# Optimization experiments

Hardware: AMD Instinct MI355X
Metric: run time of the kernel (lower is better)

The kernel has to match this reference:

```python
import jax, jax.numpy as jnp
import numpy as np

B, N, F, D, M, R, K, TOPR = 32, 1024, 10, 64, 4, 8, 20, 2
TAU = 1.0
BN_EPS = 1e-5


def setup_inputs() -> dict:
    key = jax.random.key(0)
    ks = jax.random.split(key, 20)
    s = 0.1
    p = {}
    p['data'] = jax.random.normal(ks[0], (B, N, F), jnp.float32)
    u = jnp.clip(jax.random.uniform(ks[1], (B, M), jnp.float32), 1e-6, 1.0 - 1e-6)
    p['gumbel_noise'] = -jnp.log(-jnp.log(u))
    p['W_cond'] = jax.random.normal(ks[2], (F, D), jnp.float32) * s
    p['b_cond'] = jnp.zeros((D,), jnp.float32)
    p['W_ap'] = jax.random.normal(ks[3], (D, D), jnp.float32) * s
    p['b_ap'] = jnp.zeros((D,), jnp.float32)
    p['W_av'] = jax.random.normal(ks[4], (D, 1), jnp.float32) * s
    p['W_r'] = jax.random.normal(ks[5], (D, M), jnp.float32) * s
    p['b_r'] = jnp.zeros((M,), jnp.float32)
    p['e_base'] = jax.random.normal(ks[6], (N, D), jnp.float32) * s
    p['lr_u'] = jax.random.normal(ks[7], (M, N, R), jnp.float32) * s
    p['lr_v'] = jax.random.normal(ks[8], (M, R, D), jnp.float32) * s
    p['W_gnn'] = jax.random.normal(ks[9], (F, D), jnp.float32) * s
    p['att_i'] = jax.random.normal(ks[10], (D,), jnp.float32) * s
    p['att_j'] = jax.random.normal(ks[11], (D,), jnp.float32) * s
    p['att_em_i'] = jax.random.normal(ks[12], (D,), jnp.float32) * s
    p['att_em_j'] = jax.random.normal(ks[13], (D,), jnp.float32) * s
    p['b_gnn'] = jnp.zeros((D,), jnp.float32)
    p['bn1_gamma'] = jnp.ones((D,), jnp.float32)
    p['bn1_beta'] = jnp.zeros((D,), jnp.float32)
    p['node_embed_table'] = jax.random.normal(ks[14], (N, D), jnp.float32) * s
    p['bn_out_gamma'] = jnp.ones((D,), jnp.float32)
    p['bn_out_beta'] = jnp.zeros((D,), jnp.float32)
    p['W_out'] = jax.random.normal(ks[15], (D, 1), jnp.float32) * s
    p['b_out'] = jnp.zeros((1,), jnp.float32)
    return p


def _nan(x):
    return jnp.nan_to_num(x, nan=0.0, posinf=1e4, neginf=-1e4)


def _bn(x, gamma, beta, axes):
    # BatchNorm1d in training mode: biased batch stats over `axes`.
    mu = x.mean(axes, keepdims=True)
    var = x.var(axes, keepdims=True)
    return (x - mu) * jax.lax.rsqrt(var + BN_EPS) * gamma + beta


def reference(data, gumbel_noise, W_cond, b_cond, W_ap, b_ap, W_av, W_r, b_r,
              e_base, lr_u, lr_v, W_gnn, att_i, att_j, att_em_i, att_em_j,
              b_gnn, bn1_gamma, bn1_beta, node_embed_table,
              bn_out_gamma, bn_out_beta, W_out, b_out):
    x_det = jax.lax.stop_gradient(data)                      # data.clone().detach()
    # --- condition attention pooling ---
    h_it = data @ W_cond + b_cond                            # [B,N,D]
    ah = jax.nn.leaky_relu(h_it @ W_ap + b_ap, 0.2)
    e_it = _nan((ah @ W_av)[..., 0])                         # [B,N]
    beta = jax.nn.softmax(e_it, axis=1)
    h_sys = jnp.sum(beta[..., None] * h_it, axis=1)          # [B,D]
    # --- gumbel top-k routing with straight-through ---
    pi_soft = jax.nn.softmax((h_sys @ W_r + b_r + gumbel_noise) / TAU, axis=-1)
    topv, topi = jax.lax.top_k(pi_soft, TOPR)
    pi_hard = jnp.sum(jax.nn.one_hot(topi, M, dtype=pi_soft.dtype) * topv[..., None], axis=1)
    pi_hard = pi_hard / jnp.maximum(pi_hard.sum(-1, keepdims=True), 1e-12)
    pi_t = jax.lax.stop_gradient(pi_hard - pi_soft) + pi_soft
    # --- low-rank expert prototypes -> mixed node embeddings ---
    proto = e_base[None] + jnp.einsum('mnr,mrd->mnd', lr_u, lr_v)    # [M,N,D]
    mixed = _nan(jnp.einsum('bm,mnd->bnd', pi_t, proto))             # [B,N,D]
    # --- dynamic top-k graph construction ---
    scores = _nan(jnp.einsum('bid,bjd->bij', mixed, mixed))          # [B,N,N]
    topk_vals, topk_idx = jax.lax.top_k(scores, K)                   # src nodes per dst: [B,N,K]
    topk_w = jax.nn.softmax(topk_vals, axis=-1)                      # edge weights
    # --- GAT-style layer with embedding-augmented keys, self loops re-added ---
    x_lin = x_det @ W_gnn                                            # [B,N,D]
    s_i = x_lin @ att_i + mixed @ att_em_i                           # [B,N]
    s_j = x_lin @ att_j + mixed @ att_em_j
    sj_nb = jnp.take_along_axis(s_j, topk_idx.reshape(B, N * K), axis=1).reshape(B, N, K)
    self_mask = topk_idx == jnp.arange(N)[None, :, None]             # remove_self_loops on topk edges
    alpha_nb = jnp.where(self_mask, -jnp.inf, jax.nn.leaky_relu(s_i[:, :, None] + sj_nb, 0.2))
    alpha_self = jax.nn.leaky_relu(s_i + s_j, 0.2)
    att = jax.nn.softmax(jnp.concatenate([alpha_nb, alpha_self[..., None]], axis=-1), axis=-1)
    w_nb = att[..., :K] * topk_w                                     # edge_weight modulation
    w_self = att[..., K]
    x_src = jnp.take_along_axis(x_lin, topk_idx.reshape(B, N * K)[..., None], axis=1).reshape(B, N, K, D)
    gnn = jnp.einsum('bnk,bnkd->bnd', w_nb, x_src) + w_self[..., None] * x_lin + b_gnn
    gnn = jax.nn.relu(_bn(gnn.reshape(B * N, D), bn1_gamma, bn1_beta, 0).reshape(B, N, D))
    # --- output head ---
    out = gnn * node_embed_table[None]                               # [B,N,D]
    out = jax.nn.relu(_bn(out, bn_out_gamma, bn_out_beta, (0, 1)))   # dropout = identity (eval)
    out = (out @ W_out + b_out).reshape(-1, N)                       # [B,N]
    return out, h_sys, pi_soft
```

## Files before the change

kernel.cpp:

```cpp
#include <hip/hip_runtime.h>
#include <math.h>

#define BB 32
#define NN 1024
#define FF 10
#define DD 64
#define MM 4
#define RR 8
#define KK 20
#define BNROWS (BB*NN)

#define OFF_HIT   0ull
#define OFF_XLIN  2097152ull
#define OFF_EIT   4194304ull
#define OFF_PIT   4227072ull
#define OFF_MIXED 4227200ull
#define OFF_SI    6324352ull
#define OFF_SJ    6357120ull
#define OFF_GNN   7700608ull
#define OFF_OUTP  9797760ull
#define OFF_STAT  11894912ull
#define OFF_SC    (OFF_STAT + 2560ull)

__device__ __forceinline__ float wave_sum(float v) {
    #pragma unroll
    for (int off = 32; off; off >>= 1) v += __shfl_xor(v, off);
    return v;
}
__device__ __forceinline__ float wave_max(float v) {
    #pragma unroll
    for (int off = 32; off; off >>= 1) v = fmaxf(v, __shfl_xor(v, off));
    return v;
}

__global__ __launch_bounds__(256) void k_rows(
    const float* __restrict__ data, const float* __restrict__ W_cond,
    const float* __restrict__ b_cond, const float* __restrict__ W_ap,
    const float* __restrict__ b_ap, const float* __restrict__ W_av,
    const float* __restrict__ W_gnn,
    float* __restrict__ h_it, float* __restrict__ x_lin, float* __restrict__ e_it,
    float* __restrict__ stats)
{
    if (blockIdx.x < 10) {
        int idx = blockIdx.x * 256 + threadIdx.x;
        if (idx < 2336) stats[idx] = 0.f;
    }
    int w = threadIdx.x >> 6, lane = threadIdx.x & 63;
    int r = blockIdx.x * 4 + w;
    const float* dr = data + r * FF;
    float df[FF];
    #pragma unroll
    for (int f = 0; f < FF; f++) df[f] = dr[f];
    float h = b_cond[lane], x = 0.f;
    #pragma unroll
    for (int f = 0; f < FF; f++) {
        h = fmaf(df[f], W_cond[f * DD + lane], h);
        x = fmaf(df[f], W_gnn[f * DD + lane], x);
    }
    h_it[r * DD + lane] = h;
    x_lin[r * DD + lane] = x;
    float acc = b_ap[lane];
    #pragma unroll
    for (int e2 = 0; e2 < DD; e2++)
        acc = fmaf(__shfl(h, e2), W_ap[e2 * DD + lane], acc);
    float lr = acc > 0.f ? acc : 0.2f * acc;
    float ep = wave_sum(lr * W_av[lane]);
    if (lane == 0) e_it[r] = ep;
}

__global__ __launch_bounds__(256) void k_pool2(
    const float* __restrict__ e_it, const float* __restrict__ h_it,
    float* __restrict__ num, float* __restrict__ den)
{
    int w = threadIdx.x >> 6, lane = threadIdx.x & 63;
    int b = blockIdx.x >> 3, ch = blockIdx.x & 7;
    int base = b * NN + ch * 128 + w * 32;
    float acc = 0.f, dn = 0.f;
    #pragma unroll 4
    for (int i = 0; i < 32; i++) {
        float e = e_it[base + i];
        float wgt = expf(e);
        acc = fmaf(wgt, h_it[(size_t)(base + i) * DD + lane], acc);
        dn += wgt;
    }
    __shared__ float pa[4][DD];
    __shared__ float pd[4];
    pa[w][lane] = acc;
    if (lane == 0) pd[w] = dn;
    __syncthreads();
    if (w == 0) {
        float s = pa[0][lane] + pa[1][lane] + pa[2][lane] + pa[3][lane];
        atomicAdd(&num[b * DD + lane], s);
        if (lane == 0) atomicAdd(&den[b], pd[0] + pd[1] + pd[2] + pd[3]);
    }
}

__global__ void k_route(const float* __restrict__ num, const float* __restrict__ den,
                        const float* __restrict__ W_r, const float* __restrict__ b_r,
                        const float* __restrict__ gumbel,
                        float* __restrict__ h_sys, float* __restrict__ pi_soft,
                        float* __restrict__ pi_t)
{
    int tid = threadIdx.x;
    for (int i = tid; i < BB * DD; i += 256)
        h_sys[i] = num[i] / den[i >> 6];
    if (tid >= BB) return;
    int b = tid;
    float inv = 1.0f / den[b];
    float lg[MM];
    #pragma unroll
    for (int m = 0; m < MM; m++) lg[m] = b_r[m] + gumbel[b * MM + m];
    for (int d = 0; d < DD; d++) {
        float hv = num[b * DD + d] * inv;
        #pragma unroll
        for (int m = 0; m < MM; m++) lg[m] = fmaf(hv, W_r[d * MM + m], lg[m]);
    }
    float mx = fmaxf(fmaxf(lg[0], lg[1]), fmaxf(lg[2], lg[3]));
    float s = 0.f, p[MM];
    #pragma unroll
    for (int m = 0; m < MM; m++) { p[m] = expf(lg[m] - mx); s += p[m]; }
    #pragma unroll
    for (int m = 0; m < MM; m++) { p[m] /= s; pi_soft[b * MM + m] = p[m]; }
    int i1 = 0; float v1 = p[0];
    #pragma unroll
    for (int m = 1; m < MM; m++) if (p[m] > v1) { v1 = p[m]; i1 = m; }
    int i2 = -1; float v2 = -1.f;
    #pragma unroll
    for (int m = 0; m < MM; m++) if (m != i1 && p[m] > v2) { v2 = p[m]; i2 = m; }
    float norm = fmaxf(v1 + v2, 1e-12f);
    #pragma unroll
    for (int m = 0; m < MM; m++)
        pi_t[b * MM + m] = (m == i1 ? v1 : (m == i2 ? v2 : 0.f)) / norm;
}

__global__ __launch_bounds__(256) void k_mixed(
    const float* __restrict__ e_base, const float* __restrict__ lr_u,
    const float* __restrict__ lr_v, const float* __restrict__ pi_t,
    const float* __restrict__ x_lin,
    const float* __restrict__ att_i, const float* __restrict__ att_j,
    const float* __restrict__ att_em_i, const float* __restrict__ att_em_j,
    float* __restrict__ mixed, float* __restrict__ s_i, float* __restrict__ s_j)
{
    int w = threadIdx.x >> 6, lane = threadIdx.x & 63;
    int r = blockIdx.x * 4 + w;
    int b = r >> 10, n = r & 1023;
    float LR[MM];
    #pragma unroll
    for (int m = 0; m < MM; m++) {
        float a = 0.f;
        #pragma unroll
        for (int rr = 0; rr < RR; rr++)
            a = fmaf(lr_u[(m * NN + n) * RR + rr], lr_v[(m * RR + rr) * DD + lane], a);
        LR[m] = a;
    }
    float eb = e_base[n * DD + lane];
    float mx = 0.f;
    #pragma unroll
    for (int m = 0; m < MM; m++) mx = fmaf(pi_t[b * MM + m], eb + LR[m], mx);
    mixed[(size_t)r * DD + lane] = mx;
    float x = x_lin[(size_t)r * DD + lane];
    float r1 = wave_sum(x * att_i[lane] + mx * att_em_i[lane]);
    float r2 = wave_sum(x * att_j[lane] + mx * att_em_j[lane]);
    if (lane == 0) { s_i[r] = r1; s_j[r] = r2; }
}

__global__ __launch_bounds__(256) void k_score(
    const float* __restrict__ mixed_chunk, float* __restrict__ sc)
{
    __shared__ float As[32 * 132];
    __shared__ float Bs[32 * 132];
    int t = threadIdx.x;
    int bb = blockIdx.x >> 6;
    int rr = blockIdx.x & 63;
    int it = rr >> 3, jt = rr & 7;
    int i0 = it * 128, j0 = jt * 128;
    const float* mb = mixed_chunk + (size_t)bb * NN * DD;

    int tx = t & 15, ty = t >> 4;
    float acc[8][8];
    #pragma unroll
    for (int a = 0; a < 8; a++)
        #pragma unroll
        for (int bj = 0; bj < 8; bj++) acc[a][bj] = 0.f;

    int rowi[4], qi[4], swi[4];
    #pragma unroll
    for (int c = 0; c < 4; c++) {
        int id = t + c * 256;
        rowi[c] = (id & 15) | ((id >> 7) << 4);
        qi[c] = (id >> 4) & 7;
        swi[c] = ((rowi[c] & 4) << 4) | ((rowi[c] >> 3) << 2) | (rowi[c] & 3);
    }

    float4 pa[4], pb[4];
    #pragma unroll
    for (int c = 0; c < 4; c++) {
        pa[c] = *(const float4*)(mb + (size_t)(i0 + rowi[c]) * DD + qi[c] * 4);
        pb[c] = *(const float4*)(mb + (size_t)(j0 + rowi[c]) * DD + qi[c] * 4);
    }
    for (int hh = 0; hh < 2; hh++) {
        if (hh) __syncthreads();
        #pragma unroll
        for (int c = 0; c < 4; c++) {
            int pos = qi[c] * 4 * 132 + swi[c];
            As[pos] = pa[c].x; As[pos + 132] = pa[c].y; As[pos + 264] = pa[c].z; As[pos + 396] = pa[c].w;
            Bs[pos] = pb[c].x; Bs[pos + 132] = pb[c].y; Bs[pos + 264] = pb[c].z; Bs[pos + 396] = pb[c].w;
        }
        __syncthreads();
        if (hh == 0) {
            #pragma unroll
            for (int c = 0; c < 4; c++) {
                pa[c] = *(const float4*)(mb + (size_t)(i0 + rowi[c]) * DD + 32 + qi[c] * 4);
                pb[c] = *(const float4*)(mb + (size_t)(j0 + rowi[c]) * DD + 32 + qi[c] * 4);
            }
        }
        #pragma unroll 4
        for (int d = 0; d < 32; d++) {
            float4 a0 = *(const float4*)&As[d * 132 + ty * 4];
            float4 a1 = *(const float4*)&As[d * 132 + 64 + ty * 4];
            float4 b0 = *(const float4*)&Bs[d * 132 + tx * 4];
            float4 b1 = *(const float4*)&Bs[d * 132 + 64 + tx * 4];
            float av[8] = {a0.x, a0.y, a0.z, a0.w, a1.x, a1.y, a1.z, a1.w};
            float bv[8] = {b0.x, b0.y, b0.z, b0.w, b1.x, b1.y, b1.z, b1.w};
            #pragma unroll
            for (int a = 0; a < 8; a++)
                #pragma unroll
                for (int bj = 0; bj < 8; bj++)
                    acc[a][bj] = fmaf(av[a], bv[bj], acc[a][bj]);
        }
    }

    float* out = sc + ((size_t)bb * NN + i0 + ty * 8) * NN + j0 + tx * 8;
    #pragma unroll
    for (int a = 0; a < 8; a++) {
        float4 o0 = {acc[a][0], acc[a][1], acc[a][2], acc[a][3]};
        float4 o1 = {acc[a][4], acc[a][5], acc[a][6], acc[a][7]};
        *(float4*)(out + (size_t)a * NN) = o0;
        *(float4*)(out + (size_t)a * NN + 4) = o1;
    }
}

__global__ __launch_bounds__(256) void k_selgat(
    const float* __restrict__ sc, int b0,
    const float* __restrict__ x_lin, const float* __restrict__ s_i,
    const float* __restrict__ s_j, const float* __restrict__ b_gnn,
    float* __restrict__ gnn_pre)
{
    int w = threadIdx.x >> 6, lane = threadIdx.x & 63;
    int lr = blockIdx.x * 4 + w;
    int r = b0 * NN + lr;
    int b = r >> 10, n = r & 1023;
    const float* row = sc + (size_t)lr * NN;

    unsigned uk[16];
    #pragma unroll
    for (int c = 0; c < 4; c++) {
        float4 v = *(const float4*)(row + c * 256 + lane * 4);
        float vv[4] = {v.x, v.y, v.z, v.w};
        #pragma unroll
        for (int q = 0; q < 4; q++) {
            unsigned u = __float_as_uint(vv[q]);
            uk[c * 4 + q] = u ^ (((unsigned)((int)u >> 31)) | 0x80000000u);
        }
    }
    unsigned mx = uk[0];
    #pragma unroll
    for (int i = 1; i < 16; i++) mx = uk[i] > mx ? uk[i] : mx;
    unsigned sv = mx;
    #pragma unroll
    for (int blk = 2; blk <= 64; blk <<= 1) {
        #pragma unroll
        for (int dist = blk >> 1; dist >= 1; dist >>= 1) {
            unsigned pv = (unsigned)__shfl_xor((int)sv, dist);
            bool up = (lane & blk) == 0;
            bool upper = (lane & dist) == 0;
            bool g = sv > pv;
            sv = (((g == upper) == up)) ? sv : pv;
        }
    }
    unsigned tau = (unsigned)__shfl((int)sv, 19);

    __shared__ unsigned skey[4][64];
    __shared__ int sjj[4][64];
    int base = 0;
    #pragma unroll
    for (int s = 0; s < 16; s++) {
        bool q = uk[s] >= tau;
        unsigned long long m = __ballot(q);
        if (q) {
            int pos = base + __popcll(m & ((1ull << lane) - 1ull));
            if (pos < 64) {
                skey[w][pos] = uk[s];
                sjj[w][pos] = ((s >> 2) << 8) + lane * 4 + (s & 3);
            }
        }
        base += __popcll(m);
    }
    int C = base;

    float vk = -INFINITY; int ik = 0;
    if (C <= 64) {
        unsigned ck = 0u; int cj = 0x7FFFFFFF;
        if (lane < C) { ck = skey[w][lane]; cj = sjj[w][lane]; }
        if (C <= 32) {
            #pragma unroll
            for (int blk = 2; blk <= 32; blk <<= 1)
                #pragma unroll
                for (int dist = blk >> 1; dist >= 1; dist >>= 1) {
                    unsigned pk = (unsigned)__shfl_xor((int)ck, dist);
                    int pj = __shfl_xor(cj, dist);
                    bool up = (lane & blk) == 0;
                    bool upper = (lane & dist) == 0;
                    bool g = (ck > pk) || (ck == pk && cj < pj);
                    bool keep = ((g == upper) == up);
                    ck = keep ? ck : pk; cj = keep ? cj : pj;
                }
        } else {
            #pragma unroll
            for (int blk = 2; blk <= 64; blk <<= 1)
                #pragma unroll
                for (int dist = blk >> 1; dist >= 1; dist >>= 1) {
                    unsigned pk = (unsigned)__shfl_xor((int)ck, dist);
                    int pj = __shfl_xor(cj, dist);
                    bool up = (lane & blk) == 0;
                    bool upper = (lane & dist) == 0;
                    bool g = (ck > pk) || (ck == pk && cj < pj);
                    bool keep = ((g == upper) == up);
                    ck = keep ? ck : pk; cj = keep ? cj : pj;
                }
        }
        if (lane < KK) {
            unsigned u = (ck & 0x80000000u) ? (ck ^ 0x80000000u) : ~ck;
            vk = __uint_as_float(u);
            ik = cj;
        }
    } else {
        for (int k = 0; k < KK; k++) {
            unsigned bm = uk[0]; int bsl = 0;
            #pragma unroll
            for (int i = 1; i < 16; i++) if (uk[i] > bm) { bm = uk[i]; bsl = i; }
            unsigned wm = bm;
            #pragma unroll
            for (int off = 32; off; off >>= 1) {
                unsigned tt = (unsigned)__shfl_xor((int)wm, off);
                wm = tt > wm ? tt : wm;
            }
            unsigned long long ball = __ballot(bm == wm);
            int winner = (int)__builtin_ctzll(ball);
            int slotw = __shfl(bsl, winner);
            int jw = ((slotw >> 2) << 8) + winner * 4 + (slotw & 3);
            unsigned u2 = (wm & 0x80000000u) ? (wm ^ 0x80000000u) : ~wm;
            if (lane == k) { vk = __uint_as_float(u2); ik = jw; }
            if (lane == winner) uk[bsl] = 0u;
        }
    }

    float m1 = wave_max(vk);
    float ek = (lane < KK) ? expf(vk - m1) : 0.f;
    float s1v = wave_sum(ek);
    float wk = ek / s1v;
    float si = s_i[r], sjn = s_j[r];
    float a = -INFINITY;
    if (lane < KK) {
        float sjk = s_j[(b << 10) + ik];
        float t2 = si + sjk;
        a = (ik == n) ? -INFINITY : (t2 > 0.f ? t2 : 0.2f * t2);
    }
    float ts = si + sjn;
    float aself = ts > 0.f ? ts : 0.2f * ts;
    float am = wave_max(fmaxf(a, aself));
    float ea = (lane < KK && a != -INFINITY) ? expf(a - am) : 0.f;
    float es = expf(aself - am);
    float ssum = wave_sum(ea) + es;
    float wnb = (ea / ssum) * wk;
    float wself = es / ssum;
    float acc = b_gnn[lane] + wself * x_lin[(size_t)r * DD + lane];
    #pragma unroll
    for (int k = 0; k < KK; k++) {
        int jk = __shfl(ik, k);
        float wv = __shfl(wnb, k);
        acc = fmaf(wv, x_lin[((size_t)(b << 10) + jk) * DD + lane], acc);
    }
    gnn_pre[(size_t)r * DD + lane] = acc;
}

__global__ __launch_bounds__(256) void k_stats(const float* __restrict__ src, float* __restrict__ sums)
{
    int w = threadIdx.x >> 6, lane = threadIdx.x & 63;
    __shared__ float ps[4][DD], pq[4][DD];
    float s = 0.f, q = 0.f;
    int base = blockIdx.x * 128;
    for (int i = w; i < 128; i += 4) {
        float v = src[(size_t)(base + i) * DD + lane];
        s += v; q = fmaf(v, v, q);
    }
    ps[w][lane] = s; pq[w][lane] = q;
    __syncthreads();
    if (w == 0) {
        s = ps[0][lane] + ps[1][lane] + ps[2][lane] + ps[3][lane];
        q = pq[0][lane] + pq[1][lane] + pq[2][lane] + pq[3][lane];
        atomicAdd(&sums[lane], s);
        atomicAdd(&sums[DD + lane], q);
    }
}

__global__ __launch_bounds__(256) void k_bn1(
    const float* __restrict__ gnn_pre, float* __restrict__ stats,
    const float* __restrict__ gamma, const float* __restrict__ beta,
    const float* __restrict__ net, float* __restrict__ out_pre)
{
    int tid = threadIdx.x;
    int d0 = (tid & 15) * 4;
    float mean4[4], rs4[4], bt4[4];
    #pragma unroll
    for (int k = 0; k < 4; k++) {
        float mu = stats[d0 + k] * (1.0f / BNROWS);
        float var = stats[64 + d0 + k] * (1.0f / BNROWS) - mu * mu;
        mean4[k] = mu;
        rs4[k] = rsqrtf(var + 1e-5f) * gamma[d0 + k];
        bt4[k] = beta[d0 + k];
    }
    float s4[4] = {0, 0, 0, 0}, q4[4] = {0, 0, 0, 0};
    size_t base4 = (size_t)blockIdx.x * 2048;
    #pragma unroll
    for (int i = 0; i < 8; i++) {
        size_t f4 = base4 + (size_t)i * 256 + tid;
        float4 v = ((const float4*)gnn_pre)[f4];
        int n = ((int)(f4 >> 4)) & 1023;
        float4 nv = ((const float4*)net)[(size_t)n * 16 + (tid & 15)];
        float vv[4] = {v.x, v.y, v.z, v.w};
        float nn2[4] = {nv.x, nv.y, nv.z, nv.w};
        float ov[4];
        #pragma unroll
        for (int k = 0; k < 4; k++) {
            float y = (vv[k] - mean4[k]) * rs4[k] + bt4[k];
            y = y > 0.f ? y : 0.f;
            float o = y * nn2[k];
            ov[k] = o;
            s4[k] += o;
            q4[k] = fmaf(o, o, q4[k]);
        }
        float4 o4 = {ov[0], ov[1], ov[2], ov[3]};
        ((float4*)out_pre)[f4] = o4;
    }
    __shared__ float4 ls[256], lq[256];
    ls[tid] = make_float4(s4[0], s4[1], s4[2], s4[3]);
    lq[tid] = make_float4(q4[0], q4[1], q4[2], q4[3]);
    __syncthreads();
    if (tid < 16) {
        float4 S = ls[tid], Q = lq[tid];
        #pragma unroll
        for (int rr = 1; rr < 16; rr++) {
            float4 a = ls[tid + 16 * rr], b = lq[tid + 16 * rr];
            S.x += a.x; S.y += a.y; S.z += a.z; S.w += a.w;
            Q.x += b.x; Q.y += b.y; Q.z += b.z; Q.w += b.w;
        }
        atomicAdd(&stats[128 + tid * 4 + 0], S.x);
        atomicAdd(&stats[128 + tid * 4 + 1], S.y);
        atomicAdd(&stats[128 + tid * 4 + 2], S.z);
        atomicAdd(&stats[128 + tid * 4 + 3], S.w);
        atomicAdd(&stats[192 + tid * 4 + 0], Q.x);
        atomicAdd(&stats[192 + tid * 4 + 1], Q.y);
        atomicAdd(&stats[192 + tid * 4 + 2], Q.z);
        atomicAdd(&stats[192 + tid * 4 + 3], Q.w);
    }
}

__global__ __launch_bounds__(256) void k_head(
    const float* __restrict__ out_pre, const float* __restrict__ stats,
    const float* __restrict__ gamma, const float* __restrict__ beta,
    const float* __restrict__ W_out, const float* __restrict__ b_out,
    float* __restrict__ out)
{
    int w = threadIdx.x >> 6, lane = threadIdx.x & 63;
    int r = blockIdx.x * 4 + w;
    float mean = stats[lane] * (1.0f / BNROWS);
    float var = stats[DD + lane] * (1.0f / BNROWS) - mean * mean;
    float rs = rsqrtf(var + 1e-5f);
    float y = (out_pre[(size_t)r * DD + lane] - mean) * rs * gamma[lane] + beta[lane];
    y = y > 0.f ? y : 0.f;
    float p = wave_sum(y * W_out[lane]);
    if (lane == 0) out[r] = p + b_out[0];
}

extern "C" void kernel_launch(void* const* d_in, const int* in_sizes, int n_in,
                              void* d_out, int out_size, void* d_ws, size_t ws_size,
                              hipStream_t stream)
{
    const float* data     = (const float*)d_in[0];
    const float* gumbel   = (const float*)d_in[1];
    const float* W_cond   = (const float*)d_in[2];
    const float* b_cond   = (const float*)d_in[3];
    const float* W_ap     = (const float*)d_in[4];
    const float* b_ap     = (const float*)d_in[5];
    const float* W_av     = (const float*)d_in[6];
    const float* W_r      = (const float*)d_in[7];
    const float* b_r      = (const float*)d_in[8];
    const float* e_base   = (const float*)d_in[9];
    const float* lr_u     = (const float*)d_in[10];
    const float* lr_v     = (const float*)d_in[11];
    const float* W_gnn    = (const float*)d_in[12];
    const float* att_i    = (const float*)d_in[13];
    const float* att_j    = (const float*)d_in[14];
    const float* att_em_i = (const float*)d_in[15];
    const float* att_em_j = (const float*)d_in[16];
    const float* b_gnn    = (const float*)d_in[17];
    const float* bn1_g    = (const float*)d_in[18];
    const float* bn1_b    = (const float*)d_in[19];
    const float* net      = (const float*)d_in[20];
    const float* bno_g    = (const float*)d_in[21];
    const float* bno_b    = (const float*)d_in[22];
    const float* W_out    = (const float*)d_in[23];
    const float* b_out    = (const float*)d_in[24];

    float* ws = (float*)d_ws;
    float* h_it   = ws + OFF_HIT;
    float* x_lin  = ws + OFF_XLIN;
    float* e_it   = ws + OFF_EIT;
    float* pi_t   = ws + OFF_PIT;
    float* mixed  = ws + OFF_MIXED;
    float* s_i    = ws + OFF_SI;
    float* s_j    = ws + OFF_SJ;
    float* gnn_pre = ws + OFF_GNN;
    float* out_pre = ws + OFF_OUTP;
    float* stats   = ws + OFF_STAT;
    float* pnum    = stats + 256;
    float* pden    = stats + 2304;

    float* out0    = (float*)d_out;
    float* h_sys   = out0 + BB * NN;
    float* pi_soft = out0 + BB * NN + BB * DD;

    k_rows<<<BNROWS / 4, 256, 0, stream>>>(data, W_cond, b_cond, W_ap, b_ap, W_av, W_gnn,
                                           h_it, x_lin, e_it, stats);
    k_pool2<<<BB * 8, 256, 0, stream>>>(e_it, h_it, pnum, pden);
    k_route<<<1, 256, 0, stream>>>(pnum, pden, W_r, b_r, gumbel, h_sys, pi_soft, pi_t);
    k_mixed<<<BNROWS / 4, 256, 0, stream>>>(e_base, lr_u, lr_v, pi_t, x_lin,
                                            att_i, att_j, att_em_i, att_em_j, mixed, s_i, s_j);

    size_t ws_floats = ws_size / 4;
    size_t avail = ws_floats > OFF_SC ? ws_floats - OFF_SC : 0;
    int cb = (int)(avail / (size_t)(NN * NN));
    if (cb > BB) cb = BB;
    float* sc = ws + OFF_SC;
    if (cb < 1) { cb = 2; sc = h_it; }
    for (int b0 = 0; b0 < BB; b0 += cb) {
        int c = (BB - b0) < cb ? (BB - b0) : cb;
        k_score<<<c * 64, 256, 0, stream>>>(mixed + (size_t)b0 * NN * DD, sc);
        k_selgat<<<c * 256, 256, 0, stream>>>(sc, b0, x_lin, s_i, s_j, b_gnn, gnn_pre);
    }

    k_stats<<<256, 256, 0, stream>>>(gnn_pre, stats);
    k_bn1<<<256, 256, 0, stream>>>(gnn_pre, stats, bn1_g, bn1_b, net, out_pre);
    k_head<<<BNROWS / 4, 256, 0, stream>>>(out_pre, stats + 128, bno_g, bno_b, W_out, b_out, out0);
}
```

Measured before the change: 319.8 us.

## Fuse whole pipeline into one cooperative persistent kernel with grid syncs

Replaces the sequence of separate kernel launches with a single cooperative kernel on a fixed grid of 512 blocks. Stages are separated by grid-wide syncs, and grid-stride loops process rows and tiles. BN1 statistics are now accumulated inside the selection/GAT stage instead of a separate stats pass, and the fallback path gets the same fusion. This removes launch gaps and one full read of gnn_pre, at the cost of fewer blocks per stage, lower occupancy under launch bounds of (256,2), and several grid.sync barriers.

```diff
diff --git a/kernel.cpp b/kernel.cpp
--- a/kernel.cpp
+++ b/kernel.cpp
@@ -1,5 +1,8 @@
 #include <hip/hip_runtime.h>
+#include <hip/hip_cooperative_groups.h>
 #include <math.h>
+
+namespace cg = cooperative_groups;
 
 #define BB 32
 #define NN 1024
@@ -9,6 +12,7 @@
 #define RR 8
 #define KK 20
 #define BNROWS (BB*NN)
+#define GRID 512
 
 #define OFF_HIT   0ull
 #define OFF_XLIN  2097152ull
@@ -22,6 +26,16 @@
 #define OFF_STAT  11894912ull
 #define OFF_SC    (OFF_STAT + 2560ull)
 
+struct MegaArgs {
+    const float *data, *gumbel, *W_cond, *b_cond, *W_ap, *b_ap, *W_av, *W_r, *b_r,
+                *e_base, *lr_u, *lr_v, *W_gnn, *att_i, *att_j, *att_em_i, *att_em_j,
+                *b_gnn, *bn1_g, *bn1_b, *net, *bno_g, *bno_b, *W_out, *b_out;
+    float* ws;
+    float* out0;
+    float* sc;
+    int cb;
+};
+
 __device__ __forceinline__ float wave_sum(float v) {
     #pragma unroll
     for (int off = 32; off; off >>= 1) v += __shfl_xor(v, off);
@@ -31,6 +45,442 @@
     #pragma unroll
     for (int off = 32; off; off >>= 1) v = fmaxf(v, __shfl_xor(v, off));
     return v;
+}
+
+__global__ __launch_bounds__(256, 2) void k_mega(MegaArgs a)
+{
+    cg::grid_group grid = cg::this_grid();
+    __shared__ __align__(16) float smem[8448];
+
+    int t = threadIdx.x, w = t >> 6, lane = t & 63;
+    int blk = blockIdx.x;
+    int nb = gridDim.x;
+    int nwaves = nb * 4;
+    int gw = blk * 4 + w;
+
+    float* ws      = a.ws;
+    float* h_it    = ws + OFF_HIT;
+    float* x_lin   = ws + OFF_XLIN;
+    float* e_it    = ws + OFF_EIT;
+    float* pi_t    = ws + OFF_PIT;
+    float* mixed   = ws + OFF_MIXED;
+    float* s_i     = ws + OFF_SI;
+    float* s_j     = ws + OFF_SJ;
+    float* gnn_pre = ws + OFF_GNN;
+    float* out_pre = ws + OFF_OUTP;
+    float* stats   = ws + OFF_STAT;
+    float* pnum    = stats + 256;
+    float* pden    = stats + 2304;
+    float* out0    = a.out0;
+    float* h_sys   = out0 + BB * NN;
+    float* pi_soft = out0 + BB * NN + BB * DD;
+
+    if (blk == 0)
+        for (int idx = t; idx < 2336; idx += 256) stats[idx] = 0.f;
+    for (int r = gw; r < BNROWS; r += nwaves) {
+        const float* dr = a.data + r * FF;
+        float df[FF];
+        #pragma unroll
+        for (int f = 0; f < FF; f++) df[f] = dr[f];
+        float h = a.b_cond[lane], x = 0.f;
+        #pragma unroll
+        for (int f = 0; f < FF; f++) {
+            h = fmaf(df[f], a.W_cond[f * DD + lane], h);
+            x = fmaf(df[f], a.W_gnn[f * DD + lane], x);
+        }
+        h_it[r * DD + lane] = h;
+        x_lin[r * DD + lane] = x;
+        float acc = a.b_ap[lane];
+        #pragma unroll
+        for (int e2 = 0; e2 < DD; e2++)
+            acc = fmaf(__shfl(h, e2), a.W_ap[e2 * DD + lane], acc);
+        float lr2 = acc > 0.f ? acc : 0.2f * acc;
+        float ep = wave_sum(lr2 * a.W_av[lane]);
+        if (lane == 0) e_it[r] = ep;
+    }
+    grid.sync();
+
+    for (int ch = blk; ch < 256; ch += nb) {
+        __syncthreads();
+        int b = ch >> 3, c8 = ch & 7;
+        int base = b * NN + c8 * 128 + w * 32;
+        float accp = 0.f, dn = 0.f;
+        #pragma unroll 4
+        for (int i = 0; i < 32; i++) {
+            float e = e_it[base + i];
+            float wgt = expf(e);
+            accp = fmaf(wgt, h_it[(size_t)(base + i) * DD + lane], accp);
+            dn += wgt;
+        }
+        float* pa = smem;
+        float* pd = smem + 256;
+        pa[w * 64 + lane] = accp;
+        if (lane == 0) pd[w] = dn;
+        __syncthreads();
+        if (w == 0) {
+            float s = pa[lane] + pa[64 + lane] + pa[128 + lane] + pa[192 + lane];
+            atomicAdd(&pnum[b * DD + lane], s);
+            if (lane == 0) atomicAdd(&pden[b], pd[0] + pd[1] + pd[2] + pd[3]);
+        }
+    }
+    grid.sync();
+
+    if (blk == 0) {
+        for (int i = t; i < BB * DD; i += 256)
+            h_sys[i] = pnum[i] / pden[i >> 6];
+        if (t < BB) {
+            int b = t;
+            float inv = 1.0f / pden[b];
+            float lg[MM];
+            #pragma unroll
+            for (int m = 0; m < MM; m++) lg[m] = a.b_r[m] + a.gumbel[b * MM + m];
+            for (int d = 0; d < DD; d++) {
+                float hv = pnum[b * DD + d] * inv;
+                #pragma unroll
+                for (int m = 0; m < MM; m++) lg[m] = fmaf(hv, a.W_r[d * MM + m], lg[m]);
+            }
+            float mx = fmaxf(fmaxf(lg[0], lg[1]), fmaxf(lg[2], lg[3]));
+            float s = 0.f, p[MM];
+            #pragma unroll
+            for (int m = 0; m < MM; m++) { p[m] = expf(lg[m] - mx); s += p[m]; }
+            #pragma unroll
+            for (int m = 0; m < MM; m++) { p[m] /= s; pi_soft[b * MM + m] = p[m]; }
+            int i1 = 0; float v1 = p[0];
+            #pragma unroll
+            for (int m = 1; m < MM; m++) if (p[m] > v1) { v1 = p[m]; i1 = m; }
+            int i2 = -1; float v2 = -1.f;
+            #pragma unroll
+            for (int m = 0; m < MM; m++) if (m != i1 && p[m] > v2) { v2 = p[m]; i2 = m; }
+            float norm = fmaxf(v1 + v2, 1e-12f);
+            #pragma unroll
+            for (int m = 0; m < MM; m++)
+                pi_t[b * MM + m] = (m == i1 ? v1 : (m == i2 ? v2 : 0.f)) / norm;
+        }
+    }
+    grid.sync();
+
+    for (int r = gw; r < BNROWS; r += nwaves) {
+        int b = r >> 10, n = r & 1023;
+        float LR[MM];
+        #pragma unroll
+        for (int m = 0; m < MM; m++) {
+            float ac = 0.f;
+            #pragma unroll
+            for (int rr = 0; rr < RR; rr++)
+                ac = fmaf(a.lr_u[(m * NN + n) * RR + rr], a.lr_v[(m * RR + rr) * DD + lane], ac);
+            LR[m] = ac;
+        }
+        float eb = a.e_base[n * DD + lane];
+        float mx = 0.f;
+        #pragma unroll
+        for (int m = 0; m < MM; m++) mx = fmaf(pi_t[b * MM + m], eb + LR[m], mx);
+        mixed[(size_t)r * DD + lane] = mx;
+        float x = x_lin[(size_t)r * DD + lane];
+        float r1 = wave_sum(x * a.att_i[lane] + mx * a.att_em_i[lane]);
+        float r2 = wave_sum(x * a.att_j[lane] + mx * a.att_em_j[lane]);
+        if (lane == 0) { s_i[r] = r1; s_j[r] = r2; }
+    }
+    grid.sync();
+
+    float* sc = a.sc;
+    for (int b0 = 0; b0 < BB; b0 += a.cb) {
+        int c = (BB - b0) < a.cb ? (BB - b0) : a.cb;
+
+        float* As = smem;
+        float* Bs = smem + 4224;
+        for (int tt = blk; tt < c * 64; tt += nb) {
+            int bb = tt >> 6;
+            int rr = tt & 63;
+            int it = rr >> 3, jt = rr & 7;
+            int i0 = it * 128, j0 = jt * 128;
+            const float* mb = mixed + (size_t)(b0 + bb) * NN * DD;
+
+            int tx = t & 15, ty = t >> 4;
+            float acc[8][8];
+            #pragma unroll
+            for (int aa = 0; aa < 8; aa++)
+                #pragma unroll
+                for (int bj = 0; bj < 8; bj++) acc[aa][bj] = 0.f;
+
+            int rowi[4], qi[4], swi[4];
+            #pragma unroll
+            for (int c2 = 0; c2 < 4; c2++) {
+                int id = t + c2 * 256;
+                rowi[c2] = (id & 15) | ((id >> 7) << 4);
+                qi[c2] = (id >> 4) & 7;
+                swi[c2] = ((rowi[c2] & 4) << 4) | ((rowi[c2] >> 3) << 2) | (rowi[c2] & 3);
+            }
+            float4 pa4[4], pb4[4];
+            #pragma unroll
+            for (int c2 = 0; c2 < 4; c2++) {
+                pa4[c2] = *(const float4*)(mb + (size_t)(i0 + rowi[c2]) * DD + qi[c2] * 4);
+                pb4[c2] = *(const float4*)(mb + (size_t)(j0 + rowi[c2]) * DD + qi[c2] * 4);
+            }
+            for (int hh = 0; hh < 2; hh++) {
+                __syncthreads();
+                #pragma unroll
+                for (int c2 = 0; c2 < 4; c2++) {
+                    int pos = qi[c2] * 4 * 132 + swi[c2];
+                    As[pos] = pa4[c2].x; As[pos + 132] = pa4[c2].y; As[pos + 264] = pa4[c2].z; As[pos + 396] = pa4[c2].w;
+                    Bs[pos] = pb4[c2].x; Bs[pos + 132] = pb4[c2].y; Bs[pos + 264] = pb4[c2].z; Bs[pos + 396] = pb4[c2].w;
+                }
+                __syncthreads();
+                if (hh == 0) {
+                    #pragma unroll
+                    for (int c2 = 0; c2 < 4; c2++) {
+                        pa4[c2] = *(const float4*)(mb + (size_t)(i0 + rowi[c2]) * DD + 32 + qi[c2] * 4);
+                        pb4[c2] = *(const float4*)(mb + (size_t)(j0 + rowi[c2]) * DD + 32 + qi[c2] * 4);
+                    }
+                }
+                #pragma unroll 4
+                for (int d = 0; d < 32; d++) {
+                    float4 a0 = *(const float4*)&As[d * 132 + ty * 4];
+                    float4 a1 = *(const float4*)&As[d * 132 + 64 + ty * 4];
+                    float4 b0v = *(const float4*)&Bs[d * 132 + tx * 4];
+                    float4 b1v = *(const float4*)&Bs[d * 132 + 64 + tx * 4];
+                    float av[8] = {a0.x, a0.y, a0.z, a0.w, a1.x, a1.y, a1.z, a1.w};
+                    float bv[8] = {b0v.x, b0v.y, b0v.z, b0v.w, b1v.x, b1v.y, b1v.z, b1v.w};
+                    #pragma unroll
+                    for (int aa = 0; aa < 8; aa++)
+                        #pragma unroll
+                        for (int bj = 0; bj < 8; bj++)
+                            acc[aa][bj] = fmaf(av[aa], bv[bj], acc[aa][bj]);
+                }
+            }
+            float* outp = sc + ((size_t)bb * NN + i0 + ty * 8) * NN + j0 + tx * 8;
+            #pragma unroll
+            for (int aa = 0; aa < 8; aa++) {
+                float4 o0 = {acc[aa][0], acc[aa][1], acc[aa][2], acc[aa][3]};
+                float4 o1 = {acc[aa][4], acc[aa][5], acc[aa][6], acc[aa][7]};
+                *(float4*)(outp + (size_t)aa * NN) = o0;
+                *(float4*)(outp + (size_t)aa * NN + 4) = o1;
+            }
+        }
+        grid.sync();
+
+        unsigned* skey = (unsigned*)smem;
+        int* sjjm = (int*)(smem + 256);
+        float* spart = smem + 512;
+        float sl = 0.f, ql = 0.f;
+        for (int lrow = gw; lrow < c * NN; lrow += nwaves) {
+            int gr = (b0 << 10) + lrow;
+            int b = gr >> 10, n = gr & 1023;
+            const float* row = sc + (size_t)lrow * NN;
+
+            unsigned uk[16];
+            #pragma unroll
+            for (int c2 = 0; c2 < 4; c2++) {
+                float4 v = *(const float4*)(row + c2 * 256 + lane * 4);
+                float vv[4] = {v.x, v.y, v.z, v.w};
+                #pragma unroll
+                for (int q = 0; q < 4; q++) {
+                    unsigned u = __float_as_uint(vv[q]);
+                    uk[c2 * 4 + q] = u ^ (((unsigned)((int)u >> 31)) | 0x80000000u);
+                }
+            }
+            unsigned mxk = uk[0];
+            #pragma unroll
+            for (int i = 1; i < 16; i++) mxk = uk[i] > mxk ? uk[i] : mxk;
+            unsigned sv = mxk;
+            #pragma unroll
+            for (int blk2 = 2; blk2 <= 64; blk2 <<= 1) {
+                #pragma unroll
+                for (int dist = blk2 >> 1; dist >= 1; dist >>= 1) {
+                    unsigned pv = (unsigned)__shfl_xor((int)sv, dist);
+                    bool up = (lane & blk2) == 0;
+                    bool upper = (lane & dist) == 0;
+                    bool g = sv > pv;
+                    sv = (((g == upper) == up)) ? sv : pv;
+                }
+            }
+            unsigned tau = (unsigned)__shfl((int)sv, 19);
+
+            int base = 0;
+            #pragma unroll
+            for (int s = 0; s < 16; s++) {
+                bool q = uk[s] >= tau;
+                unsigned long long m = __ballot(q);
+                if (q) {
+                    int pos = base + __popcll(m & ((1ull << lane) - 1ull));
+                    if (pos < 64) {
+                        skey[w * 64 + pos] = uk[s];
+                        sjjm[w * 64 + pos] = ((s >> 2) << 8) + lane * 4 + (s & 3);
+                    }
+                }
+                base += __popcll(m);
+            }
+            int C = base;
+
+            float vk = -INFINITY; int ik = 0;
+            if (C <= 64) {
+                unsigned ck = 0u; int cj = 0x7FFFFFFF;
+                if (lane < C) { ck = skey[w * 64 + lane]; cj = sjjm[w * 64 + lane]; }
+                if (C <= 32) {
+                    #pragma unroll
+                    for (int blk2 = 2; blk2 <= 32; blk2 <<= 1)
+                        #pragma unroll
+                        for (int dist = blk2 >> 1; dist >= 1; dist >>= 1) {
+                            unsigned pk = (unsigned)__shfl_xor((int)ck, dist);
+                            int pj = __shfl_xor(cj, dist);
+                            bool up = (lane & blk2) == 0;
+                            bool upper = (lane & dist) == 0;
+                            bool g = (ck > pk) || (ck == pk && cj < pj);
+                            bool keep = ((g == upper) == up);
+                            ck = keep ? ck : pk; cj = keep ? cj : pj;
+                        }
+                } else {
+                    #pragma unroll
+                    for (int blk2 = 2; blk2 <= 64; blk2 <<= 1)
+                        #pragma unroll
+                        for (int dist = blk2 >> 1; dist >= 1; dist >>= 1) {
+                            unsigned pk = (unsigned)__shfl_xor((int)ck, dist);
+                            int pj = __shfl_xor(cj, dist);
+                            bool up = (lane & blk2) == 0;
+                            bool upper = (lane & dist) == 0;
+                            bool g = (ck > pk) || (ck == pk && cj < pj);
+                            bool keep = ((g == upper) == up);
+                            ck = keep ? ck : pk; cj = keep ? cj : pj;
+                        }
+                }
+                if (lane < KK) {
+                    unsigned u = (ck & 0x80000000u) ? (ck ^ 0x80000000u) : ~ck;
+                    vk = __uint_as_float(u);
+                    ik = cj;
+                }
+            } else {
+                for (int k = 0; k < KK; k++) {
+                    unsigned bm = uk[0]; int bsl = 0;
+                    #pragma unroll
+                    for (int i = 1; i < 16; i++) if (uk[i] > bm) { bm = uk[i]; bsl = i; }
+                    unsigned wm = bm;
+                    #pragma unroll
+                    for (int off = 32; off; off >>= 1) {
+                        unsigned tt2 = (unsigned)__shfl_xor((int)wm, off);
+                        wm = tt2 > wm ? tt2 : wm;
+                    }
+                    unsigned long long ball = __ballot(bm == wm);
+                    int winner = (int)__builtin_ctzll(ball);
+                    int slotw = __shfl(bsl, winner);
+                    int jw = ((slotw >> 2) << 8) + winner * 4 + (slotw & 3);
+                    unsigned u2 = (wm & 0x80000000u) ? (wm ^ 0x80000000u) : ~wm;
+                    if (lane == k) { vk = __uint_as_float(u2); ik = jw; }
+                    if (lane == winner) uk[bsl] = 0u;
+                }
+            }
+
+            float m1 = wave_max(vk);
+            float ek = (lane < KK) ? expf(vk - m1) : 0.f;
+            float s1v = wave_sum(ek);
+            float wk = ek / s1v;
+            float si = s_i[gr], sjn = s_j[gr];
+            float aat = -INFINITY;
+            if (lane < KK) {
+                float sjk = s_j[(b << 10) + ik];
+                float t2 = si + sjk;
+                aat = (ik == n) ? -INFINITY : (t2 > 0.f ? t2 : 0.2f * t2);
+            }
+            float tsv = si + sjn;
+            float aself = tsv > 0.f ? tsv : 0.2f * tsv;
+            float am = wave_max(fmaxf(aat, aself));
+            float ea = (lane < KK && aat != -INFINITY) ? expf(aat - am) : 0.f;
+            float es = expf(aself - am);
+            float ssum = wave_sum(ea) + es;
+            float wnb = (ea / ssum) * wk;
+            float wself = es / ssum;
+            float accg = a.b_gnn[lane] + wself * x_lin[(size_t)gr * DD + lane];
+            #pragma unroll
+            for (int k = 0; k < KK; k++) {
+                int jk = __shfl(ik, k);
+                float wv = __shfl(wnb, k);
+                accg = fmaf(wv, x_lin[((size_t)(b << 10) + jk) * DD + lane], accg);
+            }
+            gnn_pre[(size_t)gr * DD + lane] = accg;
+            sl += accg; ql = fmaf(accg, accg, ql);
+        }
+        __syncthreads();
+        spart[w * 64 + lane] = sl;
+        spart[256 + w * 64 + lane] = ql;
+        __syncthreads();
+        if (w == 0) {
+            float S = spart[lane] + spart[64 + lane] + spart[128 + lane] + spart[192 + lane];
+            float Q = spart[256 + lane] + spart[320 + lane] + spart[384 + lane] + spart[448 + lane];
+            atomicAdd(&stats[lane], S);
+            atomicAdd(&stats[64 + lane], Q);
+        }
+        grid.sync();
+    }
+
+    {
+        int d0 = (t & 15) * 4;
+        float mean4[4], rs4[4], bt4[4];
+        #pragma unroll
+        for (int k = 0; k < 4; k++) {
+            float mu = stats[d0 + k] * (1.0f / BNROWS);
+            float var = stats[64 + d0 + k] * (1.0f / BNROWS) - mu * mu;
+            mean4[k] = mu;
+            rs4[k] = rsqrtf(var + 1e-5f) * a.bn1_g[d0 + k];
+            bt4[k] = a.bn1_b[d0 + k];
+        }
+        float s4[4] = {0, 0, 0, 0}, q4[4] = {0, 0, 0, 0};
+        for (size_t f4 = (size_t)blk * 256 + t; f4 < (size_t)BNROWS * 16; f4 += (size_t)nb * 256) {
+            float4 v = ((const float4*)gnn_pre)[f4];
+            int n = ((int)(f4 >> 4)) & 1023;
+            float4 nv = ((const float4*)a.net)[(size_t)n * 16 + (t & 15)];
+            float vv[4] = {v.x, v.y, v.z, v.w};
+            float nn2[4] = {nv.x, nv.y, nv.z, nv.w};
+            float ov[4];
+            #pragma unroll
+            for (int k = 0; k < 4; k++) {
+                float y = (vv[k] - mean4[k]) * rs4[k] + bt4[k];
+                y = y > 0.f ? y : 0.f;
+                float o = y * nn2[k];
+                ov[k] = o;
+                s4[k] += o;
+                q4[k] = fmaf(o, o, q4[k]);
+            }
+            float4 o4 = {ov[0], ov[1], ov[2], ov[3]};
+            ((float4*)out_pre)[f4] = o4;
+        }
+        float4* ls = (float4*)smem;
+        float4* lq = (float4*)(smem + 1024);
+        __syncthreads();
+        ls[t] = make_float4(s4[0], s4[1], s4[2], s4[3]);
+        lq[t] = make_float4(q4[0], q4[1], q4[2], q4[3]);
+        __syncthreads();
+        if (t < 16) {
+            float4 S = ls[t], Q = lq[t];
+            #pragma unroll
+            for (int rr = 1; rr < 16; rr++) {
+                float4 aa = ls[t + 16 * rr], bb = lq[t + 16 * rr];
+                S.x += aa.x; S.y += aa.y; S.z += aa.z; S.w += aa.w;
+                Q.x += bb.x; Q.y += bb.y; Q.z += bb.z; Q.w += bb.w;
+            }
+            atomicAdd(&stats[128 + t * 4 + 0], S.x);
+            atomicAdd(&stats[128 + t * 4 + 1], S.y);
+            atomicAdd(&stats[128 + t * 4 + 2], S.z);
+            atomicAdd(&stats[128 + t * 4 + 3], S.w);
+            atomicAdd(&stats[192 + t * 4 + 0], Q.x);
+            atomicAdd(&stats[192 + t * 4 + 1], Q.y);
+            atomicAdd(&stats[192 + t * 4 + 2], Q.z);
+            atomicAdd(&stats[192 + t * 4 + 3], Q.w);
+        }
+    }
+    grid.sync();
+
+    {
+        float mean = stats[128 + lane] * (1.0f / BNROWS);
+        float var = stats[192 + lane] * (1.0f / BNROWS) - mean * mean;
+        float rs = rsqrtf(var + 1e-5f) * a.bno_g[lane];
+        float bt = a.bno_b[lane];
+        float wo = a.W_out[lane];
+        float bo = a.b_out[0];
+        for (int r = gw; r < BNROWS; r += nwaves) {
+            float y = (out_pre[(size_t)r * DD + lane] - mean) * rs + bt;
+            y = y > 0.f ? y : 0.f;
+            float p = wave_sum(y * wo);
+            if (lane == 0) out0[r] = p + bo;
+        }
+    }
 }
 
 __global__ __launch_bounds__(256) void k_rows(
@@ -191,7 +641,6 @@
         qi[c] = (id >> 4) & 7;
         swi[c] = ((rowi[c] & 4) << 4) | ((rowi[c] >> 3) << 2) | (rowi[c] & 3);
     }
-
     float4 pa[4], pb[4];
     #pragma unroll
     for (int c = 0; c < 4; c++) {
@@ -229,7 +678,6 @@
                     acc[a][bj] = fmaf(av[a], bv[bj], acc[a][bj]);
         }
     }
-
     float* out = sc + ((size_t)bb * NN + i0 + ty * 8) * NN + j0 + tx * 8;
     #pragma unroll
     for (int a = 0; a < 8; a++) {
@@ -244,7 +692,7 @@
     const float* __restrict__ sc, int b0,
     const float* __restrict__ x_lin, const float* __restrict__ s_i,
     const float* __restrict__ s_j, const float* __restrict__ b_gnn,
-    float* __restrict__ gnn_pre)
+    float* __restrict__ gnn_pre, float* __restrict__ stats)
 {
     int w = threadIdx.x >> 6, lane = threadIdx.x & 63;
     int lr = blockIdx.x * 4 + w;
@@ -374,33 +822,24 @@
     float ssum = wave_sum(ea) + es;
     float wnb = (ea / ssum) * wk;
     float wself = es / ssum;
-    float acc = b_gnn[lane] + wself * x_lin[(size_t)r * DD + lane];
+    float accg = b_gnn[lane] + wself * x_lin[(size_t)r * DD + lane];
     #pragma unroll
     for (int k = 0; k < KK; k++) {
         int jk = __shfl(ik, k);
         float wv = __shfl(wnb, k);
-        acc = fmaf(wv, x_lin[((size_t)(b << 10) + jk) * DD + lane], acc);
-    }
-    gnn_pre[(size_t)r * DD + lane] = acc;
-}
-
-__global__ __launch_bounds__(256) void k_stats(const float* __restrict__ src, float* __restrict__ sums)
-{
-    int w = threadIdx.x >> 6, lane = threadIdx.x & 63;
-    __shared__ float ps[4][DD], pq[4][DD];
-    float s = 0.f, q = 0.f;
-    int base = blockIdx.x * 128;
-    for (int i = w; i < 128; i += 4) {
-        float v = src[(size_t)(base + i) * DD + lane];
-        s += v; q = fmaf(v, v, q);
-    }
-    ps[w][lane] = s; pq[w][lane] = q;
+        accg = fmaf(wv, x_lin[((size_t)(b << 10) + jk) * DD + lane], accg);
+    }
+    gnn_pre[(size_t)r * DD + lane] = accg;
+
+    __shared__ float spart[2][4][64];
+    spart[0][w][lane] = accg;
+    spart[1][w][lane] = accg * accg;
     __syncthreads();
     if (w == 0) {
-        s = ps[0][lane] + ps[1][lane] + ps[2][lane] + ps[3][lane];
-        q = pq[0][lane] + pq[1][lane] + pq[2][lane] + pq[3][lane];
-        atomicAdd(&sums[lane], s);
-        atomicAdd(&sums[DD + lane], q);
+        float S = spart[0][0][lane] + spart[0][1][lane] + spart[0][2][lane] + spart[0][3][lane];
+        float Q = spart[1][0][lane] + spart[1][1][lane] + spart[1][2][lane] + spart[1][3][lane];
+        atomicAdd(&stats[lane], S);
+        atomicAdd(&stats[64 + lane], Q);
     }
 }
 
@@ -487,70 +926,80 @@
                               void* d_out, int out_size, void* d_ws, size_t ws_size,
                               hipStream_t stream)
 {
-    const float* data     = (const float*)d_in[0];
-    const float* gumbel   = (const float*)d_in[1];
-    const float* W_cond   = (const float*)d_in[2];
-    const float* b_cond   = (const float*)d_in[3];
-    const float* W_ap     = (const float*)d_in[4];
-    const float* b_ap     = (const float*)d_in[5];
-    const float* W_av     = (const float*)d_in[6];
-    const float* W_r      = (const float*)d_in[7];
-    const float* b_r      = (const float*)d_in[8];
-    const float* e_base   = (const float*)d_in[9];
-    const float* lr_u     = (const float*)d_in[10];
-    const float* lr_v     = (const float*)d_in[11];
-    const float* W_gnn    = (const float*)d_in[12];
-    const float* att_i    = (const float*)d_in[13];
-    const float* att_j    = (const float*)d_in[14];
-    const float* att_em_i = (const float*)d_in[15];
-    const float* att_em_j = (const float*)d_in[16];
-    const float* b_gnn    = (const float*)d_in[17];
-    const float* bn1_g    = (const float*)d_in[18];
-    const float* bn1_b    = (const float*)d_in[19];
-    const float* net      = (const float*)d_in[20];
-    const float* bno_g    = (const float*)d_in[21];
-    const float* bno_b    = (const float*)d_in[22];
-    const float* W_out    = (const float*)d_in[23];
-    const float* b_out    = (const float*)d_in[24];
-
-    float* ws = (float*)d_ws;
-    float* h_it   = ws + OFF_HIT;
-    float* x_lin  = ws + OFF_XLIN;
-    float* e_it   = ws + OFF_EIT;
-    float* pi_t   = ws + OFF_PIT;
-    float* mixed  = ws + OFF_MIXED;
-    float* s_i    = ws + OFF_SI;
-    float* s_j    = ws + OFF_SJ;
-    float* gnn_pre = ws + OFF_GNN;
-    float* out_pre = ws + OFF_OUTP;
-    float* stats   = ws + OFF_STAT;
-    float* pnum    = stats + 256;
-    float* pden    = stats + 2304;
-
-    float* out0    = (float*)d_out;
-    float* h_sys   = out0 + BB * NN;
-    float* pi_soft = out0 + BB * NN + BB * DD;
-
-    k_rows<<<BNROWS / 4, 256, 0, stream>>>(data, W_cond, b_cond, W_ap, b_ap, W_av, W_gnn,
-                                           h_it, x_lin, e_it, stats);
-    k_pool2<<<BB * 8, 256, 0, stream>>>(e_it, h_it, pnum, pden);
-    k_route<<<1, 256, 0, stream>>>(pnum, pden, W_r, b_r, gumbel, h_sys, pi_soft, pi_t);
-    k_mixed<<<BNROWS / 4, 256, 0, stream>>>(e_base, lr_u, lr_v, pi_t, x_lin,
-                                            att_i, att_j, att_em_i, att_em_j, mixed, s_i, s_j);
+    MegaArgs a;
+    a.data     = (const float*)d_in[0];
+    a.gumbel   = (const float*)d_in[1];
+    a.W_cond   = (const float*)d_in[2];
+    a.b_cond   = (const float*)d_in[3];
+    a.W_ap     = (const float*)d_in[4];
+    a.b_ap     = (const float*)d_in[5];
+    a.W_av     = (const float*)d_in[6];
+    a.W_r      = (const float*)d_in[7];
+    a.b_r      = (const float*)d_in[8];
+    a.e_base   = (const float*)d_in[9];
+    a.lr_u     = (const float*)d_in[10];
+    a.lr_v     = (const float*)d_in[11];
+    a.W_gnn    = (const float*)d_in[12];
+    a.att_i    = (const float*)d_in[13];
+    a.att_j    = (const float*)d_in[14];
+    a.att_em_i = (const float*)d_in[15];
+    a.att_em_j = (const float*)d_in[16];
+    a.b_gnn    = (const float*)d_in[17];
+    a.bn1_g    = (const float*)d_in[18];
+    a.bn1_b    = (const float*)d_in[19];
+    a.net      = (const float*)d_in[20];
+    a.bno_g    = (const float*)d_in[21];
+    a.bno_b    = (const float*)d_in[22];
+    a.W_out    = (const float*)d_in[23];
+    a.b_out    = (const float*)d_in[24];
+    a.ws   = (float*)d_ws;
+    a.out0 = (float*)d_out;
 
     size_t ws_floats = ws_size / 4;
     size_t avail = ws_floats > OFF_SC ? ws_floats - OFF_SC : 0;
     int cb = (int)(avail / (size_t)(NN * NN));
     if (cb > BB) cb = BB;
-    float* sc = ws + OFF_SC;
-    if (cb < 1) { cb = 2; sc = h_it; }
-    for (int b0 = 0; b0 < BB; b0 += cb) {
-        int c = (BB - b0) < cb ? (BB - b0) : cb;
-        k_score<<<c * 64, 256, 0, stream>>>(mixed + (size_t)b0 * NN * DD, sc);
-        k_selgat<<<c * 256, 256, 0, stream>>>(sc, b0, x_lin, s_i, s_j, b_gnn, gnn_pre);
-    }
-
-    k_stats<<<256, 256, 0, stream>>>(gnn_pre, stats);
-    k_bn1<<<256, 256, 0, stream>>>(gnn_pre, stats, bn1_g, bn1_b, net, out_pre);
-    k_head<<<BNROWS / 4, 256, 0, stream>>>(out_pre, stats + 128, bno_g, bno_b, W_out, b_out, out0);
-}
+    float* sc = a.ws + OFF_SC;
+    if (cb < 1) { cb = 2; sc = a.ws + OFF_HIT; }
+    a.sc = sc;
+    a.cb = cb;
+
+    void* params[] = { (void*)&a };
+    hipError_t err = hipLaunchCooperativeKernel((const void*)k_mega, dim3(GRID), dim3(256),
+                                                params, 0, stream);
+    if (err != hipSuccess) {
+        float* ws = a.ws;
+        float* h_it    = ws + OFF_HIT;
+        float* x_lin   = ws + OFF_XLIN;
+        float* e_it    = ws + OFF_EIT;
+        float* pi_t    = ws + OFF_PIT;
+        float* mixed   = ws + OFF_MIXED;
+        float* s_i     = ws + OFF_SI;
+        float* s_j     = ws + OFF_SJ;
+        float* gnn_pre = ws + OFF_GNN;
+        float* out_pre = ws + OFF_OUTP;
+        float* stats   = ws + OFF_STAT;
+        float* pnum    = stats + 256;
+        float* pden    = stats + 2304;
+        float* out0    = (float*)d_out;
+        float* h_sys   = out0 + BB * NN;
+        float* pi_soft = out0 + BB * NN + BB * DD;
+
+        k_rows<<<BNROWS / 4, 256, 0, stream>>>(a.data, a.W_cond, a.b_cond, a.W_ap, a.b_ap,
+                                               a.W_av, a.W_gnn, h_it, x_lin, e_it, stats);
+        k_pool2<<<BB * 8, 256, 0, stream>>>(e_it, h_it, pnum, pden);
+        k_route<<<1, 256, 0, stream>>>(pnum, pden, a.W_r, a.b_r, a.gumbel, h_sys, pi_soft, pi_t);
+        k_mixed<<<BNROWS / 4, 256, 0, stream>>>(a.e_base, a.lr_u, a.lr_v, pi_t, x_lin,
+                                                a.att_i, a.att_j, a.att_em_i, a.att_em_j,
+                                                mixed, s_i, s_j);
+        for (int b0 = 0; b0 < BB; b0 += cb) {
+            int c = (BB - b0) < cb ? (BB - b0) : cb;
+            k_score<<<c * 64, 256, 0, stream>>>(mixed + (size_t)b0 * NN * DD, sc);
+            k_selgat<<<c * 256, 256, 0, stream>>>(sc, b0, x_lin, s_i, s_j, a.b_gnn,
+                                                  gnn_pre, stats);
+        }
+        k_bn1<<<256, 256, 0, stream>>>(gnn_pre, stats, a.bn1_g, a.bn1_b, a.net, out_pre);
+        k_head<<<BNROWS / 4, 256, 0, stream>>>(out_pre, stats + 128, a.bno_g, a.bno_b,
+                                               a.W_out, a.b_out, out0);
+    }
+}
```

Result: slower. 906.5 us (+183.5%).
